# Performance work log

Measured on AMD Instinct MI355X. Metric: run time of the kernel, lower is better.

## Reference

```python
import jax, jax.numpy as jnp
import numpy as np

N_NODES = 50000
N_EDGES = 1000000
NODE_F = 64
EDGE_F = 64
OUT_F = 128
K = 2  # matches init k=2


def setup_inputs() -> dict:
    key = jax.random.key(0)
    k1, k2, k3, k4, k5, k6 = jax.random.split(key, 6)
    node_feat = jax.random.normal(k1, (N_NODES, NODE_F), dtype=jnp.float32)
    edge_feat = jax.random.normal(k2, (N_EDGES, EDGE_F), dtype=jnp.float32)
    # nn.Linear(edge_feats*2 + node_feats, out_feats): weight [out, in], bias [out]
    W = jax.random.normal(k3, (OUT_F, 2 * EDGE_F + NODE_F), dtype=jnp.float32) * 0.05
    b = jax.random.normal(k4, (OUT_F,), dtype=jnp.float32) * 0.05
    src = jax.random.randint(k5, (N_EDGES,), 0, N_NODES, dtype=jnp.int64)
    dst = jax.random.randint(k6, (N_EDGES,), 0, N_NODES, dtype=jnp.int64)
    return {"node_feat": node_feat, "edge_feat": edge_feat, "W": W, "b": b,
            "src": src, "dst": dst}


def reference(node_feat, edge_feat, W, b, src, dst):
    N = node_feat.shape[0]
    # norm = in_degrees().clamp(min=1) ** -0.5, shape [N, 1]
    deg = jax.ops.segment_sum(jnp.ones_like(dst, dtype=node_feat.dtype), dst,
                              num_segments=N)
    norm = jnp.maximum(deg, 1.0) ** -0.5
    norm = norm[:, None]
    # DGL semantics: update_all(copy_e, sum) overwrites ndata['h'] with the
    # scatter-sum of edge data over destination nodes; apply_edges then copies
    # the (un-normalized) node 'h' back to edges via edge.src.
    e = edge_feat  # [E, EDGE_F]
    fstack = [node_feat]
    for _ in range(K):
        h = jax.ops.segment_sum(e, dst, num_segments=N)  # [N, EDGE_F]
        fstack.append(h * norm)
        e = h[src]  # apply_edges: e = src node h (un-normalized)
    rst = jnp.concatenate(fstack, axis=-1) @ W.T + b  # [N, OUT_F]
    est = rst[src]  # final apply_edges copies lin output to edges
    return rst, est
```

## Files before the change

### kernel.cpp

```cpp
#include <hip/hip_runtime.h>
#include <hip/hip_bf16.h>

#define NF 64
#define N_OUT 128
#define CAT 192

typedef __attribute__((ext_vector_type(4))) float f32x4;
typedef __attribute__((ext_vector_type(8))) short bf16x8;

__device__ inline short f2bf(float x) {
  unsigned u = __float_as_uint(x);
  unsigned r = (u + 0x7fff + ((u >> 16) & 1)) >> 16;
  return (short)r;
}

__device__ inline f32x4 sx4(f32x4 v, int m) {
  f32x4 r;
  r.x = __shfl_xor(v.x, m, 64);
  r.y = __shfl_xor(v.y, m, 64);
  r.z = __shfl_xor(v.z, m, 64);
  r.w = __shfl_xor(v.w, m, 64);
  return r;
}

__global__ __launch_bounds__(256) void deg_kernel(const int* __restrict__ dst,
                                                  int* __restrict__ deg, int n_edges) {
  int i = blockIdx.x * blockDim.x + threadIdx.x;
  int stride = gridDim.x * blockDim.x;
  for (; i < n_edges; i += stride) {
    int d = __builtin_nontemporal_load(&dst[i]);
    atomicAdd(&deg[d], 1);
  }
}

__global__ __launch_bounds__(256) void scanA_kernel(const int* __restrict__ deg,
                                                    int* __restrict__ offs,
                                                    float* __restrict__ norm,
                                                    int* __restrict__ bsum, int n) {
  int tid = threadIdx.x;
  int i = blockIdx.x * 256 + tid;
  int lane = tid & 63, wid = tid >> 6;
  int v = (i < n) ? deg[i] : 0;
  int s = v;
  #pragma unroll
  for (int o = 1; o < 64; o <<= 1) {
    int t = __shfl_up(s, o, 64);
    if (lane >= o) s += t;
  }
  __shared__ int ws[4], wb[4];
  if (lane == 63) ws[wid] = s;
  __syncthreads();
  if (tid == 0) {
    int run = 0;
    #pragma unroll
    for (int w = 0; w < 4; ++w) { wb[w] = run; run += ws[w]; }
    bsum[blockIdx.x] = run;
  }
  __syncthreads();
  if (i < n) {
    offs[i] = wb[wid] + s - v;
    norm[i] = rsqrtf(fmaxf((float)v, 1.0f));
  }
}

__global__ __launch_bounds__(256) void scanB_kernel(int* __restrict__ bsum, int nb) {
  int tid = threadIdx.x, lane = tid & 63, wid = tid >> 6;
  int v = (tid < nb) ? bsum[tid] : 0;
  int s = v;
  #pragma unroll
  for (int o = 1; o < 64; o <<= 1) {
    int t = __shfl_up(s, o, 64);
    if (lane >= o) s += t;
  }
  __shared__ int ws[4], wb[4];
  if (lane == 63) ws[wid] = s;
  __syncthreads();
  if (tid == 0) {
    int run = 0;
    #pragma unroll
    for (int w = 0; w < 4; ++w) { wb[w] = run; run += ws[w]; }
  }
  __syncthreads();
  if (tid < nb) bsum[tid] = wb[wid] + s - v;
}

__global__ __launch_bounds__(256) void scanC_kernel(int* __restrict__ offs,
                                                    const int* __restrict__ bsum, int n) {
  int i = blockIdx.x * 256 + threadIdx.x;
  if (i < n) offs[i] += bsum[blockIdx.x];
}

__global__ __launch_bounds__(256) void fill_kernel(const int* __restrict__ src,
                                                   const int* __restrict__ dst,
                                                   int* __restrict__ offs,
                                                   int2* __restrict__ csr, int n_edges) {
  int i = blockIdx.x * blockDim.x + threadIdx.x;
  int stride = gridDim.x * blockDim.x;
  for (; i < n_edges; i += stride) {
    int d = __builtin_nontemporal_load(&dst[i]);
    int s = __builtin_nontemporal_load(&src[i]);
    int p = atomicAdd(&offs[d], 1);
    csr[p] = make_int2(i, s);
  }
}

__global__ __launch_bounds__(256) void h1_kernel(const float* __restrict__ edge_feat,
                                                 const int2* __restrict__ csr,
                                                 const int* __restrict__ offs,
                                                 float* __restrict__ h1, int n_nodes) {
  int n = blockIdx.x * 4 + (threadIdx.x >> 6);
  if (n >= n_nodes) return;
  int l = threadIdx.x & 63;
  int l15 = l & 15, l4 = l >> 4;
  int kb = n ? offs[n - 1] : 0;
  int ke = offs[n];
  f32x4 acc0 = {0.f, 0.f, 0.f, 0.f}, acc1 = {0.f, 0.f, 0.f, 0.f};
  int k = kb;
  for (; k + 8 <= ke; k += 8) {
    int e0 = csr[k + l4].x;
    int e1 = csr[k + 4 + l4].x;
    f32x4 v0 = __builtin_nontemporal_load((const f32x4*)&edge_feat[(size_t)e0 * NF + l15 * 4]);
    f32x4 v1 = __builtin_nontemporal_load((const f32x4*)&edge_feat[(size_t)e1 * NF + l15 * 4]);
    acc0 += v0;
    acc1 += v1;
  }
  if (k + 4 <= ke) {
    int e = csr[k + l4].x;
    acc0 += __builtin_nontemporal_load((const f32x4*)&edge_feat[(size_t)e * NF + l15 * 4]);
    k += 4;
  }
  int rem = ke - k;
  if (l4 < rem) {
    int e = csr[k + l4].x;
    acc1 += __builtin_nontemporal_load((const f32x4*)&edge_feat[(size_t)e * NF + l15 * 4]);
  }
  f32x4 t = acc0 + acc1;
  t += sx4(t, 16);
  t += sx4(t, 32);
  if (l4 == 0) *(f32x4*)&h1[(size_t)n * NF + l15 * 4] = t;
}

__global__ __launch_bounds__(256) void h2_kernel(const float* __restrict__ h1,
                                                 const int2* __restrict__ csr,
                                                 const int* __restrict__ offs,
                                                 float* __restrict__ h2, int n_nodes) {
  int n = blockIdx.x * 4 + (threadIdx.x >> 6);
  if (n >= n_nodes) return;
  int l = threadIdx.x & 63;
  int l15 = l & 15, l4 = l >> 4;
  int kb = n ? offs[n - 1] : 0;
  int ke = offs[n];
  f32x4 acc0 = {0.f, 0.f, 0.f, 0.f}, acc1 = {0.f, 0.f, 0.f, 0.f};
  int k = kb;
  for (; k + 8 <= ke; k += 8) {
    int s0 = csr[k + l4].y;
    int s1 = csr[k + 4 + l4].y;
    acc0 += *(const f32x4*)&h1[(size_t)s0 * NF + l15 * 4];
    acc1 += *(const f32x4*)&h1[(size_t)s1 * NF + l15 * 4];
  }
  if (k + 4 <= ke) {
    int s = csr[k + l4].y;
    acc0 += *(const f32x4*)&h1[(size_t)s * NF + l15 * 4];
    k += 4;
  }
  int rem = ke - k;
  if (l4 < rem) {
    int s = csr[k + l4].y;
    acc1 += *(const f32x4*)&h1[(size_t)s * NF + l15 * 4];
  }
  f32x4 t = acc0 + acc1;
  t += sx4(t, 16);
  t += sx4(t, 32);
  if (l4 == 0) *(f32x4*)&h2[(size_t)n * NF + l15 * 4] = t;
}

__global__ __launch_bounds__(256) void gemm_kernel(const float* __restrict__ node_feat,
                                                   const float* __restrict__ h1,
                                                   const float* __restrict__ h2,
                                                   const float* __restrict__ norm,
                                                   const float* __restrict__ W,
                                                   const float* __restrict__ bias,
                                                   float* __restrict__ rst, int n_nodes) {
  __shared__ short F[32 * 200];
  int tid = threadIdx.x;
  int l = tid & 63, w = tid >> 6;
  int l15 = l & 15, l4 = l >> 4;

  bf16x8 Bf[6][2];
  #pragma unroll
  for (int c = 0; c < 2; ++c) {
    int col = w * 32 + c * 16 + l15;
    const float* wp = &W[(size_t)col * CAT];
    #pragma unroll
    for (int ks = 0; ks < 6; ++ks) {
      int k0 = ks * 32 + l4 * 8;
      bf16x8 b;
      #pragma unroll
      for (int j = 0; j < 8; ++j) b[j] = f2bf(wp[k0 + j]);
      Bf[ks][c] = b;
    }
  }
  float bias0 = bias[w * 32 + l15];
  float bias1 = bias[w * 32 + 16 + l15];

  int tiles = (n_nodes + 31) / 32;
  for (int tile = blockIdx.x; tile < tiles; tile += gridDim.x) {
    int nbase = tile * 32;
    __syncthreads();
    for (int idx = tid; idx < 768; idx += 256) {
      int m = idx / 24, q = idx - m * 24;
      int n = nbase + m;
      bf16x8 pk;
      if (n < n_nodes) {
        const float* sp;
        float scale = 1.f;
        if (q < 8)       sp = &node_feat[(size_t)n * NF + q * 8];
        else if (q < 16) { sp = &h1[(size_t)n * NF + (q - 8) * 8]; scale = norm[n]; }
        else             { sp = &h2[(size_t)n * NF + (q - 16) * 8]; scale = norm[n]; }
        f32x4 v0 = *(const f32x4*)sp;
        f32x4 v1 = *(const f32x4*)(sp + 4);
        pk[0] = f2bf(v0.x * scale); pk[1] = f2bf(v0.y * scale);
        pk[2] = f2bf(v0.z * scale); pk[3] = f2bf(v0.w * scale);
        pk[4] = f2bf(v1.x * scale); pk[5] = f2bf(v1.y * scale);
        pk[6] = f2bf(v1.z * scale); pk[7] = f2bf(v1.w * scale);
      } else {
        pk = bf16x8{0,0,0,0,0,0,0,0};
      }
      *(bf16x8*)&F[m * 200 + q * 8] = pk;
    }
    __syncthreads();
    f32x4 acc00 = {0.f,0.f,0.f,0.f}, acc01 = {0.f,0.f,0.f,0.f};
    f32x4 acc10 = {0.f,0.f,0.f,0.f}, acc11 = {0.f,0.f,0.f,0.f};
    #pragma unroll
    for (int ks = 0; ks < 6; ++ks) {
      bf16x8 a0 = *(const bf16x8*)&F[l15 * 200 + ks * 32 + l4 * 8];
      bf16x8 a1 = *(const bf16x8*)&F[(16 + l15) * 200 + ks * 32 + l4 * 8];
      acc00 = __builtin_amdgcn_mfma_f32_16x16x32_bf16(a0, Bf[ks][0], acc00, 0, 0, 0);
      acc01 = __builtin_amdgcn_mfma_f32_16x16x32_bf16(a0, Bf[ks][1], acc01, 0, 0, 0);
      acc10 = __builtin_amdgcn_mfma_f32_16x16x32_bf16(a1, Bf[ks][0], acc10, 0, 0, 0);
      acc11 = __builtin_amdgcn_mfma_f32_16x16x32_bf16(a1, Bf[ks][1], acc11, 0, 0, 0);
    }
    #pragma unroll
    for (int rt = 0; rt < 2; ++rt) {
      f32x4 ac0 = rt ? acc10 : acc00;
      f32x4 ac1 = rt ? acc11 : acc01;
      #pragma unroll
      for (int r = 0; r < 4; ++r) {
        int n = nbase + rt * 16 + l4 * 4 + r;
        if (n < n_nodes) {
          int o0 = w * 32 + l15;
          rst[(size_t)n * N_OUT + o0] = ac0[r] + bias0;
          rst[(size_t)n * N_OUT + o0 + 16] = ac1[r] + bias1;
        }
      }
    }
  }
}

__global__ __launch_bounds__(256) void est_kernel(const float* __restrict__ rst,
                                                  const int* __restrict__ src,
                                                  float* __restrict__ est, int n_edges) {
  const f32x4* r4 = (const f32x4*)rst;
  f32x4* e4 = (f32x4*)est;
  int total = n_edges * 32;
  int i = blockIdx.x * blockDim.x + threadIdx.x;
  int stride = gridDim.x * blockDim.x;
  for (; i < total; i += stride) {
    int e = i >> 5, c = i & 31;
    f32x4 v = r4[(size_t)src[e] * 32 + c];
    __builtin_nontemporal_store(v, &e4[i]);
  }
}

extern "C" void kernel_launch(void* const* d_in, const int* in_sizes, int n_in,
                              void* d_out, int out_size, void* d_ws, size_t ws_size,
                              hipStream_t stream) {
  const float* node_feat = (const float*)d_in[0];
  const float* edge_feat = (const float*)d_in[1];
  const float* W = (const float*)d_in[2];
  const float* bias = (const float*)d_in[3];
  const int* src = (const int*)d_in[4];
  const int* dst = (const int*)d_in[5];
  int n_nodes = in_sizes[0] / NF;
  int n_edges = in_sizes[4];

  size_t off = 0;
  auto take = [&](size_t bytes) -> void* {
    void* p = (char*)d_ws + off;
    off += (bytes + 255) & ~(size_t)255;
    return p;
  };
  int* deg = (int*)take((size_t)n_nodes * 4);
  int* offs = (int*)take(((size_t)n_nodes + 1) * 4);
  float* norm = (float*)take((size_t)n_nodes * 4);
  int* bsum = (int*)take(256 * 4);
  int2* csr = (int2*)take((size_t)n_edges * 8);
  float* h1 = (float*)take((size_t)n_nodes * NF * 4);
  float* h2 = (float*)take((size_t)n_nodes * NF * 4);

  float* rst = (float*)d_out;
  float* est = rst + (size_t)n_nodes * N_OUT;

  hipMemsetAsync(deg, 0, (size_t)n_nodes * 4, stream);

  deg_kernel<<<2048, 256, 0, stream>>>(dst, deg, n_edges);
  int nbs = (n_nodes + 255) / 256;
  scanA_kernel<<<nbs, 256, 0, stream>>>(deg, offs, norm, bsum, n_nodes);
  scanB_kernel<<<1, 256, 0, stream>>>(bsum, nbs);
  scanC_kernel<<<nbs, 256, 0, stream>>>(offs, bsum, n_nodes);
  fill_kernel<<<2048, 256, 0, stream>>>(src, dst, offs, csr, n_edges);
  int nb = (n_nodes + 3) / 4;
  h1_kernel<<<nb, 256, 0, stream>>>(edge_feat, csr, offs, h1, n_nodes);
  h2_kernel<<<nb, 256, 0, stream>>>(h1, csr, offs, h2, n_nodes);
  gemm_kernel<<<512, 256, 0, stream>>>(node_feat, h1, h2, norm, W, bias, rst, n_nodes);
  est_kernel<<<4096, 256, 0, stream>>>(rst, src, est, n_edges);
}
```

Measured before the change: 401.7 us.

## Fuse est scatter into GEMM via source-grouped CSR and shared-memory output tile

Builds a second CSR keyed by source node (out-degree counts, scans and fill), then has the GEMM kernel stage each 32-row output tile in shared memory. It writes rst with vector stores and scatters each row directly to all its outgoing edges in est. This removes the separate est gather kernel and its re-read of rst through src. The cost is extra atomics and CSR construction work, a larger shared-memory footprint, and edge writes that become scattered rather than sequential.

```diff
diff --git a/kernel.cpp b/kernel.cpp
--- a/kernel.cpp
+++ b/kernel.cpp
@@ -24,12 +24,14 @@
 }
 
 __global__ __launch_bounds__(256) void deg_kernel(const int* __restrict__ dst,
-                                                  int* __restrict__ deg, int n_edges) {
+                                                  const int* __restrict__ src,
+                                                  int* __restrict__ deg_in,
+                                                  int* __restrict__ deg_out, int n_edges) {
   int i = blockIdx.x * blockDim.x + threadIdx.x;
   int stride = gridDim.x * blockDim.x;
   for (; i < n_edges; i += stride) {
-    int d = __builtin_nontemporal_load(&dst[i]);
-    atomicAdd(&deg[d], 1);
+    atomicAdd(&deg_in[dst[i]], 1);
+    atomicAdd(&deg_out[src[i]], 1);
   }
 }
 
@@ -59,11 +61,13 @@
   __syncthreads();
   if (i < n) {
     offs[i] = wb[wid] + s - v;
-    norm[i] = rsqrtf(fmaxf((float)v, 1.0f));
-  }
-}
-
-__global__ __launch_bounds__(256) void scanB_kernel(int* __restrict__ bsum, int nb) {
+    if (norm) norm[i] = rsqrtf(fmaxf((float)v, 1.0f));
+  }
+}
+
+__global__ __launch_bounds__(256) void scanB_kernel(int* __restrict__ bsum_in,
+                                                    int* __restrict__ bsum_out, int nb) {
+  int* bsum = blockIdx.x ? bsum_out : bsum_in;
   int tid = threadIdx.x, lane = tid & 63, wid = tid >> 6;
   int v = (tid < nb) ? bsum[tid] : 0;
   int s = v;
@@ -84,23 +88,34 @@
   if (tid < nb) bsum[tid] = wb[wid] + s - v;
 }
 
-__global__ __launch_bounds__(256) void scanC_kernel(int* __restrict__ offs,
-                                                    const int* __restrict__ bsum, int n) {
-  int i = blockIdx.x * 256 + threadIdx.x;
-  if (i < n) offs[i] += bsum[blockIdx.x];
+__global__ __launch_bounds__(256) void scanC_kernel(int* __restrict__ offs_in,
+                                                    const int* __restrict__ bsum_in,
+                                                    int* __restrict__ offs_out,
+                                                    const int* __restrict__ bsum_out,
+                                                    int n, int nbs) {
+  int b = blockIdx.x;
+  int* offs = (b < nbs) ? offs_in : offs_out;
+  const int* bsum = (b < nbs) ? bsum_in : bsum_out;
+  int bb = (b < nbs) ? b : b - nbs;
+  int i = bb * 256 + threadIdx.x;
+  if (i < n) offs[i] += bsum[bb];
 }
 
 __global__ __launch_bounds__(256) void fill_kernel(const int* __restrict__ src,
                                                    const int* __restrict__ dst,
-                                                   int* __restrict__ offs,
-                                                   int2* __restrict__ csr, int n_edges) {
+                                                   int* __restrict__ offs_in,
+                                                   int* __restrict__ offs_out,
+                                                   int2* __restrict__ csr_in,
+                                                   int* __restrict__ csr_out, int n_edges) {
   int i = blockIdx.x * blockDim.x + threadIdx.x;
   int stride = gridDim.x * blockDim.x;
   for (; i < n_edges; i += stride) {
-    int d = __builtin_nontemporal_load(&dst[i]);
-    int s = __builtin_nontemporal_load(&src[i]);
-    int p = atomicAdd(&offs[d], 1);
-    csr[p] = make_int2(i, s);
+    int d = dst[i];
+    int s = src[i];
+    int p = atomicAdd(&offs_in[d], 1);
+    csr_in[p] = make_int2(i, s);
+    int q = atomicAdd(&offs_out[s], 1);
+    csr_out[q] = i;
   }
 }
 
@@ -180,8 +195,12 @@
                                                    const float* __restrict__ norm,
                                                    const float* __restrict__ W,
                                                    const float* __restrict__ bias,
-                                                   float* __restrict__ rst, int n_nodes) {
+                                                   const int* __restrict__ offs_out,
+                                                   const int* __restrict__ csr_out,
+                                                   float* __restrict__ rst,
+                                                   float* __restrict__ est, int n_nodes) {
   __shared__ short F[32 * 200];
+  __shared__ float R[32][132];
   int tid = threadIdx.x;
   int l = tid & 63, w = tid >> 6;
   int l15 = l & 15, l4 = l >> 4;
@@ -202,6 +221,9 @@
   }
   float bias0 = bias[w * 32 + l15];
   float bias1 = bias[w * 32 + 16 + l15];
+
+  int cc = tid & 31, g = tid >> 5;
+  f32x4* e4 = (f32x4*)est;
 
   int tiles = (n_nodes + 31) / 32;
   for (int tile = blockIdx.x; tile < tiles; tile += gridDim.x) {
@@ -246,29 +268,30 @@
       f32x4 ac1 = rt ? acc11 : acc01;
       #pragma unroll
       for (int r = 0; r < 4; ++r) {
-        int n = nbase + rt * 16 + l4 * 4 + r;
-        if (n < n_nodes) {
-          int o0 = w * 32 + l15;
-          rst[(size_t)n * N_OUT + o0] = ac0[r] + bias0;
-          rst[(size_t)n * N_OUT + o0 + 16] = ac1[r] + bias1;
-        }
+        int row = rt * 16 + l4 * 4 + r;
+        R[row][w * 32 + l15] = ac0[r] + bias0;
+        R[row][w * 32 + 16 + l15] = ac1[r] + bias1;
       }
     }
-  }
-}
-
-__global__ __launch_bounds__(256) void est_kernel(const float* __restrict__ rst,
-                                                  const int* __restrict__ src,
-                                                  float* __restrict__ est, int n_edges) {
-  const f32x4* r4 = (const f32x4*)rst;
-  f32x4* e4 = (f32x4*)est;
-  int total = n_edges * 32;
-  int i = blockIdx.x * blockDim.x + threadIdx.x;
-  int stride = gridDim.x * blockDim.x;
-  for (; i < total; i += stride) {
-    int e = i >> 5, c = i & 31;
-    f32x4 v = r4[(size_t)src[e] * 32 + c];
-    __builtin_nontemporal_store(v, &e4[i]);
+    __syncthreads();
+    for (int idx = tid; idx < 32 * 32; idx += 256) {
+      int m = idx >> 5, c = idx & 31;
+      int n = nbase + m;
+      if (n < n_nodes)
+        *(f32x4*)&rst[(size_t)n * N_OUT + c * 4] = *(const f32x4*)&R[m][c * 4];
+    }
+    for (int m = 0; m < 32; ++m) {
+      int n = nbase + m;
+      if (n >= n_nodes) break;
+      int b = n ? offs_out[n - 1] : 0;
+      int eend = offs_out[n];
+      if (b == eend) continue;
+      f32x4 v = *(const f32x4*)&R[m][cc * 4];
+      for (int j = b + g; j < eend; j += 8) {
+        int e = csr_out[j];
+        __builtin_nontemporal_store(v, &e4[(size_t)e * 32 + cc]);
+      }
+    }
   }
 }
 
@@ -290,28 +313,36 @@
     off += (bytes + 255) & ~(size_t)255;
     return p;
   };
-  int* deg = (int*)take((size_t)n_nodes * 4);
-  int* offs = (int*)take(((size_t)n_nodes + 1) * 4);
+  int* deg2 = (int*)take((size_t)n_nodes * 8);
+  int* deg_in = deg2;
+  int* deg_out = deg2 + n_nodes;
+  int* offs_in = (int*)take((size_t)n_nodes * 4);
+  int* offs_out = (int*)take((size_t)n_nodes * 4);
   float* norm = (float*)take((size_t)n_nodes * 4);
-  int* bsum = (int*)take(256 * 4);
-  int2* csr = (int2*)take((size_t)n_edges * 8);
+  int* bsum_in = (int*)take(256 * 4);
+  int* bsum_out = (int*)take(256 * 4);
+  int2* csr_in = (int2*)take((size_t)n_edges * 8);
+  int* csr_out = (int*)take((size_t)n_edges * 4);
   float* h1 = (float*)take((size_t)n_nodes * NF * 4);
   float* h2 = (float*)take((size_t)n_nodes * NF * 4);
 
   float* rst = (float*)d_out;
   float* est = rst + (size_t)n_nodes * N_OUT;
 
-  hipMemsetAsync(deg, 0, (size_t)n_nodes * 4, stream);
-
-  deg_kernel<<<2048, 256, 0, stream>>>(dst, deg, n_edges);
+  hipMemsetAsync(deg2, 0, (size_t)n_nodes * 8, stream);
+
+  deg_kernel<<<2048, 256, 0, stream>>>(dst, src, deg_in, deg_out, n_edges);
   int nbs = (n_nodes + 255) / 256;
-  scanA_kernel<<<nbs, 256, 0, stream>>>(deg, offs, norm, bsum, n_nodes);
-  scanB_kernel<<<1, 256, 0, stream>>>(bsum, nbs);
-  scanC_kernel<<<nbs, 256, 0, stream>>>(offs, bsum, n_nodes);
-  fill_kernel<<<2048, 256, 0, stream>>>(src, dst, offs, csr, n_edges);
+  scanA_kernel<<<nbs, 256, 0, stream>>>(deg_in, offs_in, norm, bsum_in, n_nodes);
+  scanA_kernel<<<nbs, 256, 0, stream>>>(deg_out, offs_out, nullptr, bsum_out, n_nodes);
+  scanB_kernel<<<2, 256, 0, stream>>>(bsum_in, bsum_out, nbs);
+  scanC_kernel<<<2 * nbs, 256, 0, stream>>>(offs_in, bsum_in, offs_out, bsum_out,
+                                            n_nodes, nbs);
+  fill_kernel<<<2048, 256, 0, stream>>>(src, dst, offs_in, offs_out,
+                                        csr_in, csr_out, n_edges);
   int nb = (n_nodes + 3) / 4;
-  h1_kernel<<<nb, 256, 0, stream>>>(edge_feat, csr, offs, h1, n_nodes);
-  h2_kernel<<<nb, 256, 0, stream>>>(h1, csr, offs, h2, n_nodes);
-  gemm_kernel<<<512, 256, 0, stream>>>(node_feat, h1, h2, norm, W, bias, rst, n_nodes);
-  est_kernel<<<4096, 256, 0, stream>>>(rst, src, est, n_edges);
-}
+  h1_kernel<<<nb, 256, 0, stream>>>(edge_feat, csr_in, offs_in, h1, n_nodes);
+  h2_kernel<<<nb, 256, 0, stream>>>(h1, csr_in, offs_in, h2, n_nodes);
+  gemm_kernel<<<512, 256, 0, stream>>>(node_feat, h1, h2, norm, W, bias,
+                                       offs_out, csr_out, rst, est, n_nodes);
+}
```

After: 475.9 us. 18.5% more time.
